# Kernel tuning notes

Measured on AMD Instinct MI355X. Metric: run time of the kernel, lower is better.

Reference implementation:

```python
import jax, jax.numpy as jnp
import numpy as np

H = 128
NH = 8
HD = H // NH  # 16
TANH_ALPHA = 10.0
LN_EPS = 1e-5


def _layer_norm(x, g, b):
    mu = jnp.mean(x, axis=-1, keepdims=True)
    var = jnp.mean((x - mu) ** 2, axis=-1, keepdims=True)
    return (x - mu) / jnp.sqrt(var + LN_EPS) * g + b


def setup_inputs() -> dict:
    key = jax.random.key(0)
    ks = jax.random.split(key, 24)
    B, N = 1024, 500

    def p(k, shape):
        return jax.random.normal(k, shape, dtype=jnp.float32) * 0.05

    inp = {
        "node_embeddings": jax.random.normal(ks[0], (B, N, H), jnp.float32),
        "graph_embeddings": jax.random.normal(ks[1], (B, H), jnp.float32),
        "first_node": jax.random.randint(ks[2], (B,), 0, N, jnp.int32),
        "current_node": jax.random.randint(ks[3], (B,), 0, N, jnp.int32),
        "mask": jax.random.randint(ks[4], (B, N), 0, 2, jnp.int32),
        # linear_first: Linear(384, 128)
        "W_first": p(ks[5], (H, 3 * H)),
        "b_first": p(ks[6], (H,)),
        # ln1 / ln2
        "g1": jnp.ones((H,), jnp.float32),
        "beta1": jnp.zeros((H,), jnp.float32),
        "g2": jnp.ones((H,), jnp.float32),
        "beta2": jnp.zeros((H,), jnp.float32),
        # LSTM(128,128) single layer, gate order i,f,g,o
        "W_ih": p(ks[7], (4 * H, H)),
        "W_hh": p(ks[8], (4 * H, H)),
        "b_ih": p(ks[9], (4 * H,)),
        "b_hh": p(ks[10], (4 * H,)),
        # attention / output projections (no bias)
        "Wq": p(ks[11], (H, H)),
        "Wk": p(ks[12], (H, H)),
        "Wv": p(ks[13], (H, H)),
        "Wproj": p(ks[14], (H, H)),
        # logitk: Linear(128,128) with bias
        "Wlk": p(ks[15], (H, H)),
        "blk": p(ks[16], (H,)),
    }
    return inp


def reference(node_embeddings, graph_embeddings, W_first, b_first, g1, beta1,
              W_ih, W_hh, b_ih, b_hh, g2, beta2, Wq, Wk, Wv, Wproj, Wlk, blk,
              first_node, current_node, mask):
    B, N, _ = node_embeddings.shape
    dt = node_embeddings.dtype

    # build_cache: K/V/logitK projections of all node embeddings
    ck = node_embeddings @ Wk.T                # [B,N,128]
    cv = node_embeddings @ Wv.T                # [B,N,128]
    lk = node_embeddings @ Wlk.T + blk         # [B,N,128]

    # context construction
    bidx = jnp.arange(B)
    first_emb = node_embeddings[bidx, first_node]    # [B,128]
    cur_emb = node_embeddings[bidx, current_node]    # [B,128]
    context = jnp.concatenate([graph_embeddings, first_emb, cur_emb], axis=1)
    context = _layer_norm(context @ W_first.T + b_first, g1, beta1)

    # single LSTM step from zero state (build_cache resets h,c to 0)
    gates = context @ W_ih.T + b_ih + b_hh           # h_prev = 0 -> no W_hh term
    i, f, g, o = jnp.split(gates, 4, axis=-1)
    c = jax.nn.sigmoid(i) * jnp.tanh(g)              # c_prev = 0
    h = jax.nn.sigmoid(o) * jnp.tanh(c)
    ctx = _layer_norm(h, g2, beta2)

    # multi-head single-query attention; note (e h) split: head is the FAST dim
    q = (ctx @ Wq.T).reshape(B, HD, NH).transpose(0, 2, 1)       # [B,h,e]
    k = ck.reshape(B, N, HD, NH).transpose(0, 3, 1, 2)           # [B,h,N,e]
    v = cv.reshape(B, N, HD, NH).transpose(0, 3, 1, 2)           # [B,h,N,e]
    maskf = mask.astype(dt)
    scores = jnp.einsum('bhe,bhne->bhn', q, k) / np.sqrt(HD) + maskf[:, None, :]
    att = jax.nn.softmax(scores, axis=-1)
    oh = jnp.einsum('bhn,bhne->bhe', att, v)                     # [B,h,e]
    att_out = oh.reshape(B, H)                                   # (h e): h slow, e fast

    context_emb = att_out @ Wproj.T                              # [B,128]
    comp = jnp.einsum('be,bne->bn', lk, context_emb[:, None, :].squeeze(1)[:, :][None].squeeze(0) if False else context_emb) if False else jnp.einsum('bne,be->bn', lk, context_emb)
    comp = comp / np.sqrt(H)
    comp = TANH_ALPHA * jnp.tanh(comp)
    out = jnp.where(mask == 1, -jnp.inf, comp)
    return out
```

## Files before the change

### kernel.cpp

```cpp
#include <hip/hip_runtime.h>
#include <math.h>

#define NBATCH 1024
#define NNODE  500
#define HDIM   128
#define NHEAD  8
#define G1K    4
#define SPLIT  8
#define CHUNK  64
#define PSTRIDE 1056
#define RSQRT_H 0.08838834764831845f
#define MASK_NEG (-1e30f)

__device__ __forceinline__ float wave_sum64(float v) {
    #pragma unroll
    for (int off = 32; off >= 1; off >>= 1) v += __shfl_xor(v, off, 64);
    return v;
}
__device__ __forceinline__ float wave_max64(float v) {
    #pragma unroll
    for (int off = 32; off >= 1; off >>= 1) v = fmaxf(v, __shfl_xor(v, off, 64));
    return v;
}

template<int G>
__device__ __forceinline__ void block_ln(float (&x)[G], const float* __restrict__ gw,
                                         const float* __restrict__ bw,
                                         int t, int lane, int wv, float (*wpart)[G])
{
    float s[G];
    #pragma unroll
    for (int g = 0; g < G; ++g) s[g] = x[g];
    #pragma unroll
    for (int off = 32; off >= 1; off >>= 1) {
        #pragma unroll
        for (int g = 0; g < G; ++g) s[g] += __shfl_xor(s[g], off, 64);
    }
    if (lane == 0) {
        #pragma unroll
        for (int g = 0; g < G; ++g) wpart[wv][g] = s[g];
    }
    __syncthreads();
    float mu[G];
    #pragma unroll
    for (int g = 0; g < G; ++g) mu[g] = (wpart[0][g] + wpart[1][g]) * (1.f/128.f);
    __syncthreads();
    #pragma unroll
    for (int g = 0; g < G; ++g) { float d = x[g] - mu[g]; s[g] = d * d; }
    #pragma unroll
    for (int off = 32; off >= 1; off >>= 1) {
        #pragma unroll
        for (int g = 0; g < G; ++g) s[g] += __shfl_xor(s[g], off, 64);
    }
    if (lane == 0) {
        #pragma unroll
        for (int g = 0; g < G; ++g) wpart[wv][g] = s[g];
    }
    __syncthreads();
    float gv = gw[t], bv = bw[t];
    #pragma unroll
    for (int g = 0; g < G; ++g) {
        float var = (wpart[0][g] + wpart[1][g]) * (1.f/128.f);
        x[g] = (x[g] - mu[g]) / sqrtf(var + 1e-5f) * gv + bv;
    }
    __syncthreads();
}

__global__ __launch_bounds__(128) void k1_context(
    const float* __restrict__ node, const float* __restrict__ graph,
    const int* __restrict__ firstn, const int* __restrict__ curn,
    const float* __restrict__ W_first, const float* __restrict__ b_first,
    const float* __restrict__ g1, const float* __restrict__ beta1,
    const float* __restrict__ W_ih, const float* __restrict__ b_ih,
    const float* __restrict__ b_hh, const float* __restrict__ g2,
    const float* __restrict__ beta2, const float* __restrict__ Wq,
    const float* __restrict__ Wk, float* __restrict__ qW_out)
{
    const int t = threadIdx.x;
    const int lane = t & 63, wv = t >> 6;
    const int b0 = blockIdx.x * G1K;
    __shared__ float ctx[G1K][384];
    __shared__ float bufB[G1K][128];
    __shared__ float wpart[2][G1K];

    #pragma unroll
    for (int g = 0; g < G1K; ++g) {
        int b = b0 + g;
        ctx[g][t]       = graph[b*HDIM + t];
        ctx[g][128 + t] = node[((size_t)b*NNODE + firstn[b])*HDIM + t];
        ctx[g][256 + t] = node[((size_t)b*NNODE + curn[b])*HDIM + t];
    }
    __syncthreads();

    float x[G1K];
    {
        float bf = b_first[t];
        #pragma unroll
        for (int g = 0; g < G1K; ++g) x[g] = bf;
        for (int j = 0; j < 384; ++j) {
            float w = W_first[t*384 + j];
            #pragma unroll
            for (int g = 0; g < G1K; ++g) x[g] += ctx[g][j] * w;
        }
    }
    block_ln<G1K>(x, g1, beta1, t, lane, wv, wpart);

    #pragma unroll
    for (int g = 0; g < G1K; ++g) bufB[g][t] = x[g];
    __syncthreads();

    float gi[G1K], gg[G1K], go[G1K];
    {
        float bi = b_ih[t]       + b_hh[t];
        float bg = b_ih[256 + t] + b_hh[256 + t];
        float bo = b_ih[384 + t] + b_hh[384 + t];
        #pragma unroll
        for (int g = 0; g < G1K; ++g) { gi[g] = bi; gg[g] = bg; go[g] = bo; }
        for (int j = 0; j < 128; ++j) {
            float wi = W_ih[(size_t)t*128 + j];
            float wg = W_ih[(size_t)(256 + t)*128 + j];
            float wo = W_ih[(size_t)(384 + t)*128 + j];
            #pragma unroll
            for (int g = 0; g < G1K; ++g) {
                float v = bufB[g][j];
                gi[g] += v * wi; gg[g] += v * wg; go[g] += v * wo;
            }
        }
    }
    #pragma unroll
    for (int g = 0; g < G1K; ++g) {
        float ig = 1.f / (1.f + expf(-gi[g]));
        float cc = ig * tanhf(gg[g]);
        float og = 1.f / (1.f + expf(-go[g]));
        x[g] = og * tanhf(cc);
    }
    block_ln<G1K>(x, g2, beta2, t, lane, wv, wpart);

    #pragma unroll
    for (int g = 0; g < G1K; ++g) bufB[g][t] = x[g];
    __syncthreads();

    float q8[G1K];
    #pragma unroll
    for (int g = 0; g < G1K; ++g) q8[g] = 0.f;
    for (int j = 0; j < 128; ++j) {
        float w = Wq[t*128 + j];
        #pragma unroll
        for (int g = 0; g < G1K; ++g) q8[g] += bufB[g][j] * w;
    }
    __syncthreads();
    #pragma unroll
    for (int g = 0; g < G1K; ++g) bufB[g][t] = q8[g];
    __syncthreads();

    for (int h = 0; h < NHEAD; ++h) {
        float a[G1K];
        #pragma unroll
        for (int g = 0; g < G1K; ++g) a[g] = 0.f;
        for (int e = 0; e < 16; ++e) {
            float w = Wk[(e*8 + h)*HDIM + t];
            #pragma unroll
            for (int g = 0; g < G1K; ++g) a[g] += bufB[g][e*8 + h] * w;
        }
        #pragma unroll
        for (int g = 0; g < G1K; ++g)
            qW_out[((size_t)(b0 + g)*NHEAD + h)*HDIM + t] = 0.25f * a[g];
    }
}

__global__ __launch_bounds__(256) void k2a_partial(
    const float* __restrict__ node, const int* __restrict__ mask,
    const float* __restrict__ qW, float* __restrict__ part)
{
    const int b = blockIdx.x >> 3;
    const int s = blockIdx.x & (SPLIT - 1);
    const int tid = threadIdx.x;
    const int lane = tid & 63;
    const int wave = tid >> 6;
    const int n0 = s * CHUNK;

    __shared__ float4 s_tile[CHUNK*32];
    __shared__ __align__(16) float s_qw[NHEAD*HDIM];
    __shared__ float  s_p[NHEAD*CHUNK];

    ((float4*)s_qw)[tid] = ((const float4*)(qW + (size_t)b*NHEAD*HDIM))[tid];

    const float* nodeb = node + (size_t)b*NNODE*HDIM;
    float* pbase = part + (size_t)blockIdx.x * PSTRIDE;

    #pragma unroll
    for (int i = 0; i < 8; ++i) {
        int idx = i*256 + tid;
        int r = idx >> 5, qq = idx & 31;
        int gn = n0 + r;
        float4 v = make_float4(0.f, 0.f, 0.f, 0.f);
        if (gn < NNODE) v = *(const float4*)(nodeb + (size_t)gn*HDIM + qq*4);
        s_tile[r*32 + (qq ^ (r & 31))] = v;
    }
    __syncthreads();

    {
        const int sn = tid & 63;
        const int hp = tid >> 6;
        float s0 = 0.f, s1 = 0.f;
        const int rb = sn*32, sw = sn & 31;
        const float4* qa = (const float4*)(s_qw + hp*HDIM);
        const float4* qb = (const float4*)(s_qw + (hp + 4)*HDIM);
        #pragma unroll 8
        for (int qq = 0; qq < 32; ++qq) {
            float4 nv = s_tile[rb + (qq ^ sw)];
            float4 av = qa[qq];
            float4 bv = qb[qq];
            s0 += nv.x*av.x + nv.y*av.y + nv.z*av.z + nv.w*av.w;
            s1 += nv.x*bv.x + nv.y*bv.y + nv.z*bv.z + nv.w*bv.w;
        }
        int gn = n0 + sn;
        if (gn < NNODE) {
            float mf = (float)mask[(size_t)b*NNODE + gn];
            s0 += mf; s1 += mf;
        } else { s0 = -INFINITY; s1 = -INFINITY; }
        s_p[hp*64 + sn] = s0;
        s_p[(hp + 4)*64 + sn] = s1;
    }
    __syncthreads();

    for (int hh = wave; hh < NHEAD; hh += 4) {
        float sv = s_p[hh*64 + lane];
        float mx = wave_max64(sv);
        float pv = (mx == -INFINITY) ? 0.f : __expf(sv - mx);
        s_p[hh*64 + lane] = pv;
        float sm = wave_sum64(pv);
        if (lane == 0) {
            pbase[hh]     = mx;
            pbase[8 + hh] = sm;
        }
    }
    __syncthreads();

    const int sg = tid >> 5;
    const int aq = tid & 31;
    float4 acc[NHEAD];
    #pragma unroll
    for (int h = 0; h < NHEAD; ++h) acc[h] = make_float4(0.f, 0.f, 0.f, 0.f);
    #pragma unroll
    for (int j = 0; j < 8; ++j) {
        int n = sg*8 + j;
        float4 nv = s_tile[n*32 + (aq ^ (n & 31))];
        #pragma unroll
        for (int h = 0; h < NHEAD; ++h) {
            float p = s_p[h*64 + n];
            acc[h].x += p*nv.x; acc[h].y += p*nv.y;
            acc[h].z += p*nv.z; acc[h].w += p*nv.w;
        }
    }
    __syncthreads();
    #pragma unroll
    for (int h = 0; h < NHEAD; ++h) s_tile[(sg*8 + h)*32 + aq] = acc[h];
    __syncthreads();
    {
        const int h2 = tid >> 5, q2 = tid & 31;
        float4 tot = make_float4(0.f, 0.f, 0.f, 0.f);
        #pragma unroll
        for (int ss = 0; ss < 8; ++ss) {
            float4 v = s_tile[(ss*8 + h2)*32 + q2];
            tot.x += v.x; tot.y += v.y; tot.z += v.z; tot.w += v.w;
        }
        *(float4*)(pbase + 16 + h2*HDIM + q2*4) = tot;
    }
}

__global__ __launch_bounds__(256) void k2b_reduce(
    const float* __restrict__ part, const float* __restrict__ Wv,
    const float* __restrict__ Wproj, const float* __restrict__ Wlk,
    const float* __restrict__ blk, float* __restrict__ wce_out,
    float* __restrict__ bias_out)
{
    const int b = blockIdx.x;
    const int tid = threadIdx.x;
    __shared__ __align__(16) float s_an[NHEAD*HDIM];
    __shared__ float s_ao[HDIM], s_ce[HDIM];

    {
        const int h = tid >> 5, q = tid & 31;
        const float* pb = part + (size_t)b*SPLIT*PSTRIDE;
        float m[SPLIT], l[SPLIT];
        float gm = -INFINITY;
        #pragma unroll
        for (int s = 0; s < SPLIT; ++s) {
            m[s] = pb[s*PSTRIDE + h];
            l[s] = pb[s*PSTRIDE + 8 + h];
            gm = fmaxf(gm, m[s]);
        }
        float lsum = 0.f;
        float4 tot = make_float4(0.f, 0.f, 0.f, 0.f);
        #pragma unroll
        for (int s = 0; s < SPLIT; ++s) {
            float f = __expf(m[s] - gm);
            lsum += l[s] * f;
            float4 v = *(const float4*)(pb + s*PSTRIDE + 16 + h*HDIM + q*4);
            tot.x += f*v.x; tot.y += f*v.y; tot.z += f*v.z; tot.w += f*v.w;
        }
        float inv = 1.f / lsum;
        tot.x *= inv; tot.y *= inv; tot.z *= inv; tot.w *= inv;
        *(float4*)(s_an + h*HDIM + q*4) = tot;
    }
    __syncthreads();

    if (tid < HDIM) {
        const int c = tid, h = c >> 4, e = c & 15;
        const int row = e*8 + h;
        float oh = 0.f;
        for (int d = 0; d < HDIM; ++d) oh += s_an[h*HDIM + d] * Wv[row*HDIM + d];
        s_ao[c] = oh;
    }
    __syncthreads();
    if (tid < HDIM) {
        const int c = tid;
        float ce = 0.f;
        for (int j = 0; j < HDIM; ++j) ce += s_ao[j] * Wproj[c*HDIM + j];
        s_ce[c] = ce;
    }
    __syncthreads();
    if (tid < HDIM) {
        const int d = tid;
        float w = 0.f;
        for (int c = 0; c < HDIM; ++c) w += s_ce[c] * Wlk[c*HDIM + d];
        wce_out[(size_t)b*HDIM + d] = w * RSQRT_H;
        if (d == 0) {
            float bb = 0.f;
            for (int c = 0; c < HDIM; ++c) bb += s_ce[c] * blk[c];
            bias_out[b] = bb * RSQRT_H;
        }
    }
}

__global__ __launch_bounds__(256) void k2_flash_mono(
    const float* __restrict__ node, const int* __restrict__ mask,
    const float* __restrict__ qW, const float* __restrict__ Wv,
    const float* __restrict__ Wproj, const float* __restrict__ Wlk,
    const float* __restrict__ blk, float* __restrict__ wce_out,
    float* __restrict__ bias_out)
{
    const int b = blockIdx.x;
    const int tid = threadIdx.x;
    const int lane = tid & 63;
    const int wave = tid >> 6;

    __shared__ float4 s_tile[64*32];
    __shared__ __align__(16) float s_qw[NHEAD*HDIM];
    __shared__ float  s_p[NHEAD*64];
    __shared__ float  s_m[NHEAD], s_l[NHEAD], s_c[NHEAD];
    __shared__ float  s_ao[HDIM], s_ce[HDIM];

    ((float4*)s_qw)[tid] = ((const float4*)(qW + (size_t)b*NHEAD*HDIM))[tid];
    if (tid < NHEAD) { s_m[tid] = -INFINITY; s_l[tid] = 0.f; }

    float4 acc[NHEAD];
    #pragma unroll
    for (int h = 0; h < NHEAD; ++h) acc[h] = make_float4(0.f, 0.f, 0.f, 0.f);

    const int sn = tid & 63;
    const int hp = tid >> 6;
    const int sg = tid >> 5;
    const int aq = tid & 31;
    const float* nodeb = node + (size_t)b*NNODE*HDIM;

    for (int tile = 0; tile < 8; ++tile) {
        const int base = tile*64;
        #pragma unroll
        for (int i = 0; i < 8; ++i) {
            int idx = i*256 + tid;
            int r = idx >> 5, qq = idx & 31;
            int gn = base + r;
            float4 v = make_float4(0.f, 0.f, 0.f, 0.f);
            if (gn < NNODE) v = *(const float4*)(nodeb + (size_t)gn*HDIM + qq*4);
            s_tile[r*32 + (qq ^ (r & 31))] = v;
        }
        __syncthreads();
        {
            float s0 = 0.f, s1 = 0.f;
            const int rb = sn*32, sw = sn & 31;
            const float4* qa = (const float4*)(s_qw + hp*HDIM);
            const float4* qb = (const float4*)(s_qw + (hp + 4)*HDIM);
            #pragma unroll 8
            for (int qq = 0; qq < 32; ++qq) {
                float4 nv = s_tile[rb + (qq ^ sw)];
                float4 av = qa[qq];
                float4 bv = qb[qq];
                s0 += nv.x*av.x + nv.y*av.y + nv.z*av.z + nv.w*av.w;
                s1 += nv.x*bv.x + nv.y*bv.y + nv.z*bv.z + nv.w*bv.w;
            }
            int gn = base + sn;
            if (gn < NNODE) {
                float mf = (float)mask[(size_t)b*NNODE + gn];
                s0 += mf; s1 += mf;
            } else { s0 = -INFINITY; s1 = -INFINITY; }
            s_p[hp*64 + sn] = s0;
            s_p[(hp + 4)*64 + sn] = s1;
        }
        __syncthreads();
        for (int hh = wave; hh < NHEAD; hh += 4) {
            float sv = s_p[hh*64 + lane];
            float mx = wave_max64(sv);
            float mO = s_m[hh];
            float mN = fmaxf(mO, mx);
            float pv = __expf(sv - mN);
            s_p[hh*64 + lane] = pv;
            float sm = wave_sum64(pv);
            if (lane == 0) {
                float corr = __expf(mO - mN);
                s_c[hh] = corr;
                s_l[hh] = s_l[hh]*corr + sm;
                s_m[hh] = mN;
            }
        }
        __syncthreads();
        {
            #pragma unroll
            for (int h = 0; h < NHEAD; ++h) {
                float c = s_c[h];
                acc[h].x *= c; acc[h].y *= c; acc[h].z *= c; acc[h].w *= c;
            }
            #pragma unroll
            for (int j = 0; j < 8; ++j) {
                int n = sg*8 + j;
                float4 nv = s_tile[n*32 + (aq ^ (n & 31))];
                #pragma unroll
                for (int h = 0; h < NHEAD; ++h) {
                    float p = s_p[h*64 + n];
                    acc[h].x += p*nv.x; acc[h].y += p*nv.y;
                    acc[h].z += p*nv.z; acc[h].w += p*nv.w;
                }
            }
        }
        __syncthreads();
    }
    #pragma unroll
    for (int h = 0; h < NHEAD; ++h) s_tile[(sg*8 + h)*32 + aq] = acc[h];
    __syncthreads();
    {
        const int h2 = tid >> 5, q2 = tid & 31;
        float4 tot = make_float4(0.f, 0.f, 0.f, 0.f);
        #pragma unroll
        for (int s = 0; s < 8; ++s) {
            float4 v = s_tile[(s*8 + h2)*32 + q2];
            tot.x += v.x; tot.y += v.y; tot.z += v.z; tot.w += v.w;
        }
        float inv = 1.f / s_l[h2];
        tot.x *= inv; tot.y *= inv; tot.z *= inv; tot.w *= inv;
        ((float4*)s_qw)[h2*32 + q2] = tot;
    }
    __syncthreads();
    if (tid < HDIM) {
        const int c = tid, h = c >> 4, e = c & 15;
        const int row = e*8 + h;
        float oh = 0.f;
        for (int d = 0; d < HDIM; ++d) oh += s_qw[h*HDIM + d] * Wv[row*HDIM + d];
        s_ao[c] = oh;
    }
    __syncthreads();
    if (tid < HDIM) {
        const int c = tid;
        float ce = 0.f;
        for (int j = 0; j < HDIM; ++j) ce += s_ao[j] * Wproj[c*HDIM + j];
        s_ce[c] = ce;
    }
    __syncthreads();
    if (tid < HDIM) {
        const int d = tid;
        float w = 0.f;
        for (int c = 0; c < HDIM; ++c) w += s_ce[c] * Wlk[c*HDIM + d];
        wce_out[(size_t)b*HDIM + d] = w * RSQRT_H;
        if (d == 0) {
            float bb = 0.f;
            for (int c = 0; c < HDIM; ++c) bb += s_ce[c] * blk[c];
            bias_out[b] = bb * RSQRT_H;
        }
    }
}

__global__ __launch_bounds__(256) void k3_out(
    const float* __restrict__ node, const int* __restrict__ mask,
    const float* __restrict__ wce, const float* __restrict__ biasv,
    float* __restrict__ out)
{
    const int slot = (int)((blockIdx.x*256u + threadIdx.x) >> 5);
    const int q = threadIdx.x & 31;
    const int b = slot / NNODE;
    const float4 nv = *(const float4*)(node + (size_t)slot*HDIM + q*4);
    const float4 wv = *(const float4*)(wce + (size_t)b*HDIM + q*4);
    float p = nv.x*wv.x + nv.y*wv.y + nv.z*wv.z + nv.w*wv.w;
    #pragma unroll
    for (int off = 16; off >= 1; off >>= 1) p += __shfl_xor(p, off, 32);
    if (q == 0) {
        float v = 10.f * tanhf(p + biasv[b]);
        out[slot] = (mask[slot] == 1) ? MASK_NEG : v;
    }
}

extern "C" void kernel_launch(void* const* d_in, const int* in_sizes, int n_in,
                              void* d_out, int out_size, void* d_ws, size_t ws_size,
                              hipStream_t stream) {
    const float* node    = (const float*)d_in[0];
    const float* graph   = (const float*)d_in[1];
    const int*   firstn  = (const int*)d_in[2];
    const int*   curn    = (const int*)d_in[3];
    const int*   mask    = (const int*)d_in[4];
    const float* W_first = (const float*)d_in[5];
    const float* b_first = (const float*)d_in[6];
    const float* g1      = (const float*)d_in[7];
    const float* beta1   = (const float*)d_in[8];
    const float* g2      = (const float*)d_in[9];
    const float* beta2   = (const float*)d_in[10];
    const float* W_ih    = (const float*)d_in[11];
    const float* b_ih    = (const float*)d_in[13];
    const float* b_hh    = (const float*)d_in[14];
    const float* Wq      = (const float*)d_in[15];
    const float* Wk      = (const float*)d_in[16];
    const float* Wv      = (const float*)d_in[17];
    const float* Wproj   = (const float*)d_in[18];
    const float* Wlk     = (const float*)d_in[19];
    const float* blk     = (const float*)d_in[20];
    float* out = (float*)d_out;

    float* qW    = (float*)d_ws;
    float* wce   = qW + (size_t)NBATCH*NHEAD*HDIM;
    float* biasv = wce + (size_t)NBATCH*HDIM;
    float* part  = biasv + NBATCH;
    const size_t need = ((size_t)NBATCH*NHEAD*HDIM + (size_t)NBATCH*HDIM + NBATCH
                         + (size_t)NBATCH*SPLIT*PSTRIDE) * sizeof(float);

    k1_context<<<NBATCH/G1K, 128, 0, stream>>>(node, graph, firstn, curn,
        W_first, b_first, g1, beta1, W_ih, b_ih, b_hh, g2, beta2, Wq, Wk, qW);
    if (ws_size >= need) {
        k2a_partial<<<NBATCH*SPLIT, 256, 0, stream>>>(node, mask, qW, part);
        k2b_reduce<<<NBATCH, 256, 0, stream>>>(part, Wv, Wproj, Wlk, blk,
            wce, biasv);
    } else {
        k2_flash_mono<<<NBATCH, 256, 0, stream>>>(node, mask, qW, Wv, Wproj,
            Wlk, blk, wce, biasv);
    }
    k3_out<<<(NBATCH*NNODE)/8, 256, 0, stream>>>(node, mask, wce, biasv, out);
}
```

Baseline: 216.3 us.

## Double-buffer node tiles with async global-to-LDS loads and online softmax

The partial-attention kernel now uses 2 blocks per batch instead of 8. Each block walks 4 chunks of 64 nodes, keeping a running max, sum and rescaled accumulator (online softmax). The next chunk is staged into a second LDS buffer with global_load_lds while the current chunk is being computed, with the swizzle moved to the global address side. The aim is to hide global memory latency and cut the per-block setup cost. In exchange there is less grid parallelism, extra rescaling work, and a reliance on the async LDS loads being waited on correctly at the barriers.

```diff
diff --git a/kernel.cpp b/kernel.cpp
--- a/kernel.cpp
+++ b/kernel.cpp
@@ -6,7 +6,8 @@
 #define HDIM   128
 #define NHEAD  8
 #define G1K    4
-#define SPLIT  8
+#define SPLIT  2
+#define CPB    4
 #define CHUNK  64
 #define PSTRIDE 1056
 #define RSQRT_H 0.08838834764831845f
@@ -21,6 +22,12 @@
     #pragma unroll
     for (int off = 32; off >= 1; off >>= 1) v = fmaxf(v, __shfl_xor(v, off, 64));
     return v;
+}
+
+__device__ __forceinline__ void gload_lds16(const float* g, float4* l) {
+    __builtin_amdgcn_global_load_lds(
+        (const __attribute__((address_space(1))) unsigned int*)g,
+        (__attribute__((address_space(3))) unsigned int*)l, 16, 0, 0);
 }
 
 template<int G>
@@ -168,101 +175,135 @@
     }
 }
 
-__global__ __launch_bounds__(256) void k2a_partial(
+__global__ __launch_bounds__(256) void k2a_pipe(
     const float* __restrict__ node, const int* __restrict__ mask,
     const float* __restrict__ qW, float* __restrict__ part)
 {
-    const int b = blockIdx.x >> 3;
+    const int b = blockIdx.x >> 1;
     const int s = blockIdx.x & (SPLIT - 1);
     const int tid = threadIdx.x;
     const int lane = tid & 63;
     const int wave = tid >> 6;
-    const int n0 = s * CHUNK;
-
-    __shared__ float4 s_tile[CHUNK*32];
+    const int nbase = s * (CPB * CHUNK);
+
+    __shared__ float4 bufs[2][CHUNK*32];
     __shared__ __align__(16) float s_qw[NHEAD*HDIM];
     __shared__ float  s_p[NHEAD*CHUNK];
-
+    __shared__ float  s_m[NHEAD], s_l[NHEAD], s_c[NHEAD];
+
+    const float* nodeb = node + (size_t)b*NNODE*HDIM;
+
+    auto stage = [&](float4* buf, int ck) {
+        const int base = nbase + ck*CHUNK;
+        #pragma unroll
+        for (int i = 0; i < 8; ++i) {
+            int slot = i*256 + tid;
+            int r = slot >> 5, qp = slot & 31;
+            int gn = base + r;
+            if (gn < NNODE) {
+                const float* g = nodeb + (size_t)gn*HDIM + ((qp ^ (r & 31)) << 2);
+                gload_lds16(g, &buf[slot]);
+            }
+        }
+        int nval = NNODE - base;
+        if (nval < CHUNK) {
+            for (int slot = tid; slot < CHUNK*32; slot += 256)
+                if ((slot >> 5) >= nval) buf[slot] = make_float4(0.f,0.f,0.f,0.f);
+        }
+    };
+
+    stage(bufs[0], 0);
     ((float4*)s_qw)[tid] = ((const float4*)(qW + (size_t)b*NHEAD*HDIM))[tid];
-
-    const float* nodeb = node + (size_t)b*NNODE*HDIM;
-    float* pbase = part + (size_t)blockIdx.x * PSTRIDE;
-
-    #pragma unroll
-    for (int i = 0; i < 8; ++i) {
-        int idx = i*256 + tid;
-        int r = idx >> 5, qq = idx & 31;
-        int gn = n0 + r;
-        float4 v = make_float4(0.f, 0.f, 0.f, 0.f);
-        if (gn < NNODE) v = *(const float4*)(nodeb + (size_t)gn*HDIM + qq*4);
-        s_tile[r*32 + (qq ^ (r & 31))] = v;
-    }
-    __syncthreads();
-
-    {
-        const int sn = tid & 63;
-        const int hp = tid >> 6;
-        float s0 = 0.f, s1 = 0.f;
-        const int rb = sn*32, sw = sn & 31;
-        const float4* qa = (const float4*)(s_qw + hp*HDIM);
-        const float4* qb = (const float4*)(s_qw + (hp + 4)*HDIM);
-        #pragma unroll 8
-        for (int qq = 0; qq < 32; ++qq) {
-            float4 nv = s_tile[rb + (qq ^ sw)];
-            float4 av = qa[qq];
-            float4 bv = qb[qq];
-            s0 += nv.x*av.x + nv.y*av.y + nv.z*av.z + nv.w*av.w;
-            s1 += nv.x*bv.x + nv.y*bv.y + nv.z*bv.z + nv.w*bv.w;
-        }
-        int gn = n0 + sn;
-        if (gn < NNODE) {
-            float mf = (float)mask[(size_t)b*NNODE + gn];
-            s0 += mf; s1 += mf;
-        } else { s0 = -INFINITY; s1 = -INFINITY; }
-        s_p[hp*64 + sn] = s0;
-        s_p[(hp + 4)*64 + sn] = s1;
-    }
-    __syncthreads();
-
-    for (int hh = wave; hh < NHEAD; hh += 4) {
-        float sv = s_p[hh*64 + lane];
-        float mx = wave_max64(sv);
-        float pv = (mx == -INFINITY) ? 0.f : __expf(sv - mx);
-        s_p[hh*64 + lane] = pv;
-        float sm = wave_sum64(pv);
-        if (lane == 0) {
-            pbase[hh]     = mx;
-            pbase[8 + hh] = sm;
-        }
-    }
-    __syncthreads();
-
+    if (tid < NHEAD) { s_m[tid] = -INFINITY; s_l[tid] = 0.f; }
+
+    float4 acc[NHEAD];
+    #pragma unroll
+    for (int h = 0; h < NHEAD; ++h) acc[h] = make_float4(0.f, 0.f, 0.f, 0.f);
+
+    const int sn = tid & 63;
+    const int hp = tid >> 6;
     const int sg = tid >> 5;
     const int aq = tid & 31;
-    float4 acc[NHEAD];
-    #pragma unroll
-    for (int h = 0; h < NHEAD; ++h) acc[h] = make_float4(0.f, 0.f, 0.f, 0.f);
-    #pragma unroll
-    for (int j = 0; j < 8; ++j) {
-        int n = sg*8 + j;
-        float4 nv = s_tile[n*32 + (aq ^ (n & 31))];
-        #pragma unroll
-        for (int h = 0; h < NHEAD; ++h) {
-            float p = s_p[h*64 + n];
-            acc[h].x += p*nv.x; acc[h].y += p*nv.y;
-            acc[h].z += p*nv.z; acc[h].w += p*nv.w;
-        }
-    }
-    __syncthreads();
-    #pragma unroll
-    for (int h = 0; h < NHEAD; ++h) s_tile[(sg*8 + h)*32 + aq] = acc[h];
+
+    __syncthreads();
+
+    for (int ck = 0; ck < CPB; ++ck) {
+        float4* A = bufs[ck & 1];
+        if (ck + 1 < CPB) stage(bufs[(ck + 1) & 1], ck + 1);
+        const int base = nbase + ck*CHUNK;
+
+        {
+            float s0 = 0.f, s1 = 0.f;
+            const int rb = sn*32, sw = sn & 31;
+            const float4* qa = (const float4*)(s_qw + hp*HDIM);
+            const float4* qb = (const float4*)(s_qw + (hp + 4)*HDIM);
+            #pragma unroll 8
+            for (int qq = 0; qq < 32; ++qq) {
+                float4 nv = A[rb + (qq ^ sw)];
+                float4 av = qa[qq];
+                float4 bv = qb[qq];
+                s0 += nv.x*av.x + nv.y*av.y + nv.z*av.z + nv.w*av.w;
+                s1 += nv.x*bv.x + nv.y*bv.y + nv.z*bv.z + nv.w*bv.w;
+            }
+            int gn = base + sn;
+            if (gn < NNODE) {
+                float mf = (float)mask[(size_t)b*NNODE + gn];
+                s0 += mf; s1 += mf;
+            } else { s0 = -INFINITY; s1 = -INFINITY; }
+            s_p[hp*64 + sn] = s0;
+            s_p[(hp + 4)*64 + sn] = s1;
+        }
+        __syncthreads();
+
+        for (int hh = wave; hh < NHEAD; hh += 4) {
+            float sv = s_p[hh*64 + lane];
+            float mx = wave_max64(sv);
+            float mO = s_m[hh];
+            float mN = fmaxf(mO, mx);
+            float pv = __expf(sv - mN);
+            s_p[hh*64 + lane] = pv;
+            float sm = wave_sum64(pv);
+            if (lane == 0) {
+                float corr = __expf(mO - mN);
+                s_c[hh] = corr;
+                s_l[hh] = s_l[hh]*corr + sm;
+                s_m[hh] = mN;
+            }
+        }
+        __syncthreads();
+
+        {
+            #pragma unroll
+            for (int h = 0; h < NHEAD; ++h) {
+                float c = s_c[h];
+                acc[h].x *= c; acc[h].y *= c; acc[h].z *= c; acc[h].w *= c;
+            }
+            #pragma unroll
+            for (int j = 0; j < 8; ++j) {
+                int n = sg*8 + j;
+                float4 nv = A[n*32 + (aq ^ (n & 31))];
+                #pragma unroll
+                for (int h = 0; h < NHEAD; ++h) {
+                    float p = s_p[h*64 + n];
+                    acc[h].x += p*nv.x; acc[h].y += p*nv.y;
+                    acc[h].z += p*nv.z; acc[h].w += p*nv.w;
+                }
+            }
+        }
+        __syncthreads();
+    }
+
+    float* pbase = part + (size_t)blockIdx.x * PSTRIDE;
+    #pragma unroll
+    for (int h = 0; h < NHEAD; ++h) bufs[0][(sg*8 + h)*32 + aq] = acc[h];
+    if (tid < NHEAD) { pbase[tid] = s_m[tid]; pbase[8 + tid] = s_l[tid]; }
     __syncthreads();
     {
         const int h2 = tid >> 5, q2 = tid & 31;
         float4 tot = make_float4(0.f, 0.f, 0.f, 0.f);
         #pragma unroll
         for (int ss = 0; ss < 8; ++ss) {
-            float4 v = s_tile[(ss*8 + h2)*32 + q2];
+            float4 v = bufs[0][(ss*8 + h2)*32 + q2];
             tot.x += v.x; tot.y += v.y; tot.z += v.z; tot.w += v.w;
         }
         *(float4*)(pbase + 16 + h2*HDIM + q2*4) = tot;
@@ -533,7 +574,7 @@
     k1_context<<<NBATCH/G1K, 128, 0, stream>>>(node, graph, firstn, curn,
         W_first, b_first, g1, beta1, W_ih, b_ih, b_hh, g2, beta2, Wq, Wk, qW);
     if (ws_size >= need) {
-        k2a_partial<<<NBATCH*SPLIT, 256, 0, stream>>>(node, mask, qW, part);
+        k2a_pipe<<<NBATCH*SPLIT, 256, 0, stream>>>(node, mask, qW, part);
         k2b_reduce<<<NBATCH, 256, 0, stream>>>(part, Wv, Wproj, Wlk, blk,
             wce, biasv);
     } else {
```

After: 213.8 us. No clear change (-1.1%).
